# Optimization experiments

Measured on AMD Instinct MI355X. Metric: run time of the kernel, lower is better.

Reference implementation:

```python
import jax, jax.numpy as jnp
import numpy as np

N = 100000  # nodes
E = 320000  # edges
G = 64      # graphs in the batch


def setup_inputs() -> dict:
    key = jax.random.key(0)
    ks = jax.random.split(key, 16)
    inp = {
        "x": jax.random.normal(ks[0], (N, 512), dtype=jnp.float32),
        "edge_index": jax.random.randint(ks[1], (2, E), 0, N, dtype=jnp.int64),
        "batch": jnp.sort(jax.random.randint(ks[2], (N,), 0, G, dtype=jnp.int64)),
    }
    # GCNConv weights (in, out) and biases, Glorot-ish scale
    dims = [(512, 256), (256, 128), (128, 64), (64, 32)]
    for i, (din, dout) in enumerate(dims):
        inp[f"w{i+1}"] = jax.random.normal(ks[3 + i], (din, dout), dtype=jnp.float32) / np.sqrt(din)
        inp[f"b{i+1}"] = jnp.zeros((dout,), dtype=jnp.float32)
    inp["lw1"] = jax.random.normal(ks[8], (32, 16), dtype=jnp.float32) / np.sqrt(32.0)
    inp["lb1"] = jnp.zeros((16,), dtype=jnp.float32)
    inp["lw2"] = jax.random.normal(ks[9], (16, 2), dtype=jnp.float32) / np.sqrt(16.0)
    inp["lb2"] = jnpp = jnp.zeros((2,), dtype=jnp.float32)
    return inp


def _gcn_conv(h_in, w, b, src, dst, norm, n):
    # x' = D^-1/2 (A+I) D^-1/2 (X W) + b   (PyG GCNConv default)
    h = h_in @ w                                  # [N, out]
    msg = h[src] * norm[:, None]                  # gather + scale over edges(+self-loops)
    out = jax.ops.segment_sum(msg, dst, num_segments=n)  # scatter-add
    return out + b


def reference(x, edge_index, batch, w1, b1, w2, b2, w3, b3, w4, b4, lw1, lb1, lw2, lb2):
    n = x.shape[0]
    loop = jnp.arange(n, dtype=edge_index.dtype)
    src = jnp.concatenate([edge_index[0], loop])  # add self-loops
    dst = jnp.concatenate([edge_index[1], loop])
    # symmetric normalization: deg counted at dst (col) including self-loops
    deg = jax.ops.segment_sum(jnp.ones_like(dst, dtype=x.dtype), dst, num_segments=n)
    dinv = jnp.where(deg > 0, 1.0 / jnp.sqrt(deg), 0.0)
    norm = dinv[src] * dinv[dst]                  # [E+N]

    h = jax.nn.relu(_gcn_conv(x, w1, b1, src, dst, norm, n))
    h = jax.nn.relu(_gcn_conv(h, w2, b2, src, dst, norm, n))
    h = jax.nn.relu(_gcn_conv(h, w3, b3, src, dst, norm, n))
    h = _gcn_conv(h, w4, b4, src, dst, norm, n)   # [N, 32]

    # global mean pool over graphs
    sums = jax.ops.segment_sum(h, batch, num_segments=G)
    cnt = jax.ops.segment_sum(jnp.ones((n,), dtype=h.dtype), batch, num_segments=G)
    pooled = sums / jnp.maximum(cnt, 1.0)[:, None]  # [G, 32]

    # dropout p=0.8 is identity in eval mode
    out = jax.nn.relu(pooled @ lw1 + lb1) @ lw2 + lb2  # [G, 2]
    return out
```

## Files before the change

### kernel.cpp

```cpp
#include <hip/hip_runtime.h>
#include <cstdint>
#include <cstddef>


typedef __attribute__((ext_vector_type(8))) short s16x8;
typedef __attribute__((ext_vector_type(4))) float f32x4;

__device__ __forceinline__ short2 split2(float f) {
    union { float f; unsigned u; } c; c.f = f;
    short hi = (short)(c.u >> 16);
    union { unsigned u; float f; } h; h.u = c.u & 0xffff0000u;
    union { float f; unsigned u; } r; r.f = f - h.f;
    short lo = (short)(r.u >> 16);
    return make_short2(hi, lo);
}

__device__ __forceinline__ void gload16(const void* g, void* l) {
    __builtin_amdgcn_global_load_lds(
        (const __attribute__((address_space(1))) unsigned int*)g,
        (__attribute__((address_space(3))) unsigned int*)l, 16, 0, 0);
}


__global__ void k_split_x(const float* __restrict__ x, long total8,
                          unsigned short* __restrict__ xh, unsigned short* __restrict__ xl) {
    long i = (long)blockIdx.x * blockDim.x + threadIdx.x;
    long stride = (long)gridDim.x * blockDim.x;
    for (; i < total8; i += stride) {
        const float4* p = (const float4*)(x + i * 8);
        float4 a = p[0], b = p[1];
        float v[8] = {a.x, a.y, a.z, a.w, b.x, b.y, b.z, b.w};
        s16x8 h, l;
#pragma unroll
        for (int j = 0; j < 8; ++j) { short2 q = split2(v[j]); h[j] = q.x; l[j] = q.y; }
        *(s16x8*)(xh + i * 8) = h;
        *(s16x8*)(xl + i * 8) = l;
    }
}


__global__ void k_count(const int* __restrict__ dst, int E, int* __restrict__ cnt) {
    int e = blockIdx.x * blockDim.x + threadIdx.x;
    if (e < E) atomicAdd(&cnt[dst[e]], 1);
}

__global__ void k_dinv(const int* __restrict__ cnt, int n, float* __restrict__ dinv) {
    int i = blockIdx.x * blockDim.x + threadIdx.x;
    if (i < n) dinv[i] = rsqrtf((float)(cnt[i] + 1));
}

__global__ void k_scan_sums(const int* __restrict__ cnt, int n, int* __restrict__ bsum) {
    __shared__ int s[256];
    int t = threadIdx.x;
    int base = blockIdx.x * 4096 + t * 16;
    int sum = 0;
#pragma unroll
    for (int j = 0; j < 16; ++j) { int i = base + j; if (i < n) sum += cnt[i]; }
    s[t] = sum;
    __syncthreads();
    for (int off = 128; off > 0; off >>= 1) {
        if (t < off) s[t] += s[t + off];
        __syncthreads();
    }
    if (t == 0) bsum[blockIdx.x] = s[0];
}

__global__ void k_scan_offsets(const int* __restrict__ bsum, int nb,
                               int* __restrict__ boff, int* __restrict__ totalp) {
    int t = threadIdx.x;
    int v = (t < nb) ? bsum[t] : 0;
    int x = v;
    for (int off = 1; off < 64; off <<= 1) {
        int y = __shfl_up(x, off);
        if (t >= off) x += y;
    }
    if (t < nb) boff[t] = x - v;
    if (t == 63) *totalp = x;
}

__global__ void k_scan_final(const int* __restrict__ cnt, int n,
                             const int* __restrict__ boff, int* __restrict__ row_ptr) {
    __shared__ int s[256];
    int t = threadIdx.x;
    int base = blockIdx.x * 4096 + t * 16;
    int v[16]; int sum = 0;
#pragma unroll
    for (int j = 0; j < 16; ++j) { int i = base + j; v[j] = (i < n) ? cnt[i] : 0; sum += v[j]; }
    s[t] = sum;
    __syncthreads();
    for (int off = 1; off < 256; off <<= 1) {
        int y = (t >= off) ? s[t - off] : 0;
        __syncthreads();
        s[t] += y;
        __syncthreads();
    }
    int run = boff[blockIdx.x] + ((t == 0) ? 0 : s[t - 1]);
#pragma unroll
    for (int j = 0; j < 16; ++j) {
        int i = base + j;
        if (i < n) row_ptr[i] = run;
        run += v[j];
    }
}

__global__ void k_fill(const int* __restrict__ src, const int* __restrict__ dst, int E,
                       const int* __restrict__ row_ptr, int* __restrict__ cursor,
                       int* __restrict__ csr_src) {
    int e = blockIdx.x * blockDim.x + threadIdx.x;
    if (e >= E) return;
    int d = dst[e];
    int p = atomicAdd(&cursor[d], 1);
    csr_src[row_ptr[d] + p] = src[e];
}


__global__ void k_split_w(const float* __restrict__ w, int N, int total, int kshift,
                          unsigned short* __restrict__ th, unsigned short* __restrict__ tl) {
    int idx = blockIdx.x * blockDim.x + threadIdx.x;
    if (idx >= total) return;
    int nn = idx >> kshift;
    int k  = idx & ((1 << kshift) - 1);
    short2 p = split2(w[(size_t)k * N + nn]);
    th[idx] = (unsigned short)p.x;
    tl[idx] = (unsigned short)p.y;
}


template <int FN>
__global__ __launch_bounds__(256)
void k_gemm(const unsigned short* __restrict__ Ah, const unsigned short* __restrict__ Al,
            const unsigned short* __restrict__ Bth, const unsigned short* __restrict__ Btl,
            float* __restrict__ C, int M, int K, int N) {
    constexpr int FM = 4;
    constexpr int BM = 128;
    constexpr int BN = 2 * FN * 16;
    constexpr int BK = 32;
    __shared__ char sAh[BM * 64], sAl[BM * 64];
    __shared__ char sBh[BN * 64], sBl[BN * 64];

    const int tid  = threadIdx.x;
    const int lane = tid & 63;
    const int w    = tid >> 6;
    const int wm   = w & 1;
    const int wn   = w >> 1;
    const int brow = blockIdx.y * BM;
    const int bcol = blockIdx.x * BN;
    const int l15  = lane & 15;
    const int kb   = (lane >> 4) * 16;

    f32x4 acc[FM][FN];
#pragma unroll
    for (int i = 0; i < FM; ++i)
#pragma unroll
        for (int j = 0; j < FN; ++j) acc[i][j] = (f32x4){0.f, 0.f, 0.f, 0.f};

    const int KT = K / BK;
    for (int t = 0; t < KT; ++t) {
        const int k0 = t * BK;

#pragma unroll
        for (int u = 0; u < 4; ++u) {
            int id = w + u * 4;
            int hi = (id < 8) ? 1 : 0;
            int s  = hi ? id : id - 8;
            int p  = s * 64 + lane;
            int kq = (p ^ ((p >> 3) & 3)) & 3;
            int row = p >> 2;
            const unsigned short* gs = (hi ? Ah : Al) + (size_t)(brow + row) * K + k0 + kq * 8;
            gload16(gs, (hi ? sAh : sAl) + s * 1024);
        }
#pragma unroll
        for (int u = 0; u < BN / 32; ++u) {
            int id = w + u * 4;
            int hi = (id < BN / 16) ? 1 : 0;
            int s  = hi ? id : id - BN / 16;
            int p  = s * 64 + lane;
            int kq = (p ^ ((p >> 3) & 3)) & 3;
            int col = p >> 2;
            const unsigned short* gs = (hi ? Bth : Btl) + (size_t)(bcol + col) * K + k0 + kq * 8;
            gload16(gs, (hi ? sBh : sBl) + s * 1024);
        }
        __syncthreads();

        s16x8 fah[FM], fam[FM];
#pragma unroll
        for (int i = 0; i < FM; ++i) {
            int row = wm * 64 + i * 16 + l15;
            int o = row * 64 + (kb ^ (((row >> 1) & 3) << 4));
            fah[i] = *(const s16x8*)(sAh + o);
            fam[i] = *(const s16x8*)(sAl + o);
        }
#pragma unroll
        for (int j = 0; j < FN; ++j) {
            int col = wn * FN * 16 + j * 16 + l15;
            int o = col * 64 + (kb ^ (((col >> 1) & 3) << 4));
            s16x8 fbh = *(const s16x8*)(sBh + o);
            s16x8 fbm = *(const s16x8*)(sBl + o);
#pragma unroll
            for (int i = 0; i < FM; ++i) {
                acc[i][j] = __builtin_amdgcn_mfma_f32_16x16x32_bf16(fah[i], fbh, acc[i][j], 0, 0, 0);
                acc[i][j] = __builtin_amdgcn_mfma_f32_16x16x32_bf16(fam[i], fbh, acc[i][j], 0, 0, 0);
                acc[i][j] = __builtin_amdgcn_mfma_f32_16x16x32_bf16(fah[i], fbm, acc[i][j], 0, 0, 0);
            }
        }
        __syncthreads();
    }

#pragma unroll
    for (int i = 0; i < FM; ++i) {
#pragma unroll
        for (int r = 0; r < 4; ++r) {
            int row = brow + wm * 64 + i * 16 + (lane >> 4) * 4 + r;
            if (row >= M) continue;
#pragma unroll
            for (int j = 0; j < FN; ++j) {
                int col = bcol + wn * FN * 16 + j * 16 + l15;
                C[(size_t)row * N + col] = acc[i][j][r];
            }
        }
    }
}


__global__ void k_agg_split(const float4* __restrict__ h, const int* __restrict__ row_ptr,
                            const int* __restrict__ csr_src, const float* __restrict__ dinv,
                            const float* __restrict__ bias,
                            unsigned short* __restrict__ oh, unsigned short* __restrict__ ol,
                            int n, int f_shift) {
    int idx = blockIdx.x * blockDim.x + threadIdx.x;
    int dout4 = 1 << f_shift;
    int total = n << f_shift;
    if (idx >= total) return;
    int i = idx >> f_shift;
    int f = idx & (dout4 - 1);

    float di = dinv[i];
    float4 hv = h[(size_t)i * dout4 + f];
    float4 acc;
    acc.x = hv.x * di; acc.y = hv.y * di; acc.z = hv.z * di; acc.w = hv.w * di;

    int s0 = row_ptr[i], s1 = row_ptr[i + 1];
    for (int e = s0; e < s1; ++e) {
        int s = csr_src[e];
        float ds = dinv[s];
        float4 v = h[(size_t)s * dout4 + f];
        acc.x += v.x * ds; acc.y += v.y * ds; acc.z += v.z * ds; acc.w += v.w * ds;
    }
    const float4* b4 = (const float4*)bias;
    float4 b = b4[f];
    float4 o;
    o.x = fmaxf(acc.x * di + b.x, 0.f);
    o.y = fmaxf(acc.y * di + b.y, 0.f);
    o.z = fmaxf(acc.z * di + b.z, 0.f);
    o.w = fmaxf(acc.w * di + b.w, 0.f);

    short2 p0 = split2(o.x), p1 = split2(o.y), p2 = split2(o.z), p3 = split2(o.w);
    size_t base = ((size_t)i << f_shift << 2) + f * 4;
    *(ushort4*)(oh + base) = make_ushort4((unsigned short)p0.x, (unsigned short)p1.x,
                                          (unsigned short)p2.x, (unsigned short)p3.x);
    *(ushort4*)(ol + base) = make_ushort4((unsigned short)p0.y, (unsigned short)p1.y,
                                          (unsigned short)p2.y, (unsigned short)p3.y);
}


__global__ void k_agg(const float4* __restrict__ h, const int* __restrict__ row_ptr,
                      const int* __restrict__ csr_src, const float* __restrict__ dinv,
                      const float* __restrict__ bias, float4* __restrict__ out,
                      int n, int f_shift) {
    int idx = blockIdx.x * blockDim.x + threadIdx.x;
    int dout4 = 1 << f_shift;
    int total = n << f_shift;
    if (idx >= total) return;
    int i = idx >> f_shift;
    int f = idx & (dout4 - 1);

    float di = dinv[i];
    float4 hv = h[(size_t)i * dout4 + f];
    float4 acc;
    acc.x = hv.x * di; acc.y = hv.y * di; acc.z = hv.z * di; acc.w = hv.w * di;

    int s0 = row_ptr[i], s1 = row_ptr[i + 1];
    for (int e = s0; e < s1; ++e) {
        int s = csr_src[e];
        float ds = dinv[s];
        float4 v = h[(size_t)s * dout4 + f];
        acc.x += v.x * ds; acc.y += v.y * ds; acc.z += v.z * ds; acc.w += v.w * ds;
    }
    const float4* b4 = (const float4*)bias;
    float4 b = b4[f];
    float4 o;
    o.x = acc.x * di + b.x;
    o.y = acc.y * di + b.y;
    o.z = acc.z * di + b.z;
    o.w = acc.w * di + b.w;
    out[(size_t)i * dout4 + f] = o;
}


__global__ void k_pool(const float* __restrict__ h, const int* __restrict__ batch,
                       int n, float* __restrict__ pooled) {
    int g = blockIdx.x;
    int start, end;
    {
        int lo = 0, hi = n;
        while (lo < hi) { int mid = (lo + hi) >> 1; if (batch[mid] < g) lo = mid + 1; else hi = mid; }
        start = lo;
        lo = start; hi = n;
        while (lo < hi) { int mid = (lo + hi) >> 1; if (batch[mid] < g + 1) lo = mid + 1; else hi = mid; }
        end = lo;
    }
    int f = threadIdx.x & 31;
    int sub = threadIdx.x >> 5;
    float s = 0.f;
    for (int i = start + sub; i < end; i += 8) s += h[(size_t)i * 32 + f];
    __shared__ float red[8][32];
    red[sub][f] = s;
    __syncthreads();
    if (sub == 0) {
        float t = 0.f;
#pragma unroll
        for (int k = 0; k < 8; ++k) t += red[k][f];
        int c = end - start;
        pooled[g * 32 + f] = t / (float)(c > 0 ? c : 1);
    }
}


__global__ void k_mlp(const float* __restrict__ pooled, const float* __restrict__ lw1,
                      const float* __restrict__ lb1, const float* __restrict__ lw2,
                      const float* __restrict__ lb2, float* __restrict__ out, int g_count) {
    int g = threadIdx.x;
    if (g >= g_count) return;
    float p[32];
#pragma unroll
    for (int k = 0; k < 32; ++k) p[k] = pooled[g * 32 + k];
    float hmid[16];
#pragma unroll
    for (int j = 0; j < 16; ++j) {
        float s = lb1[j];
#pragma unroll
        for (int k = 0; k < 32; ++k) s += p[k] * lw1[k * 16 + j];
        hmid[j] = fmaxf(s, 0.f);
    }
#pragma unroll
    for (int o = 0; o < 2; ++o) {
        float s = lb2[o];
#pragma unroll
        for (int k = 0; k < 16; ++k) s += hmid[k] * lw2[k * 2 + o];
        out[g * 2 + o] = s;
    }
}


extern "C" void kernel_launch(void* const* d_in, const int* in_sizes, int n_in,
                              void* d_out, int out_size, void* d_ws, size_t ws_size,
                              hipStream_t stream) {
    const float* x     = (const float*)d_in[0];
    const int*   ei    = (const int*)d_in[1];
    const int*   batch = (const int*)d_in[2];
    const float* w1 = (const float*)d_in[3];  const float* b1 = (const float*)d_in[4];
    const float* w2 = (const float*)d_in[5];  const float* b2 = (const float*)d_in[6];
    const float* w3 = (const float*)d_in[7];  const float* b3 = (const float*)d_in[8];
    const float* w4 = (const float*)d_in[9];  const float* b4 = (const float*)d_in[10];
    const float* lw1 = (const float*)d_in[11]; const float* lb1 = (const float*)d_in[12];
    const float* lw2 = (const float*)d_in[13]; const float* lb2 = (const float*)d_in[14];
    float* out = (float*)d_out;

    const int n = in_sizes[0] / 512;
    const int E = in_sizes[1] / 2;
    const int G = 64;

    const int* src = ei;
    const int* dst = ei + E;

    char* ws = (char*)d_ws;
    size_t off = 0;
    auto alloc = [&](size_t bytes) -> void* {
        void* p = ws + off;
        off = (off + bytes + 255) & ~((size_t)255);
        return p;
    };
    float*          bufA = (float*)alloc((size_t)n * 256 * sizeof(float));
    unsigned short* xh   = (unsigned short*)alloc((size_t)n * 512 * 2);
    unsigned short* xl   = (unsigned short*)alloc((size_t)n * 512 * 2);
    unsigned short* pAh  = (unsigned short*)alloc((size_t)n * 256 * 2);
    unsigned short* pAl  = (unsigned short*)alloc((size_t)n * 256 * 2);
    int*   cnt     = (int*)alloc((size_t)n * sizeof(int));
    int*   row_ptr = (int*)alloc((size_t)(n + 1) * sizeof(int));
    int*   cursor  = (int*)alloc((size_t)n * sizeof(int));
    int*   csr     = (int*)alloc((size_t)E * sizeof(int));
    float* dinv    = (float*)alloc((size_t)n * sizeof(float));
    float* pooled  = (float*)alloc((size_t)G * 32 * sizeof(float));
    int*   bsum    = (int*)alloc(64 * sizeof(int));
    int*   boff    = (int*)alloc(64 * sizeof(int));
    unsigned short* w1h = (unsigned short*)alloc(256 * 512 * 2);
    unsigned short* w1l = (unsigned short*)alloc(256 * 512 * 2);
    unsigned short* w2h = (unsigned short*)alloc(128 * 256 * 2);
    unsigned short* w2l = (unsigned short*)alloc(128 * 256 * 2);
    unsigned short* w3h = (unsigned short*)alloc(64 * 128 * 2);
    unsigned short* w3l = (unsigned short*)alloc(64 * 128 * 2);
    unsigned short* w4h = (unsigned short*)alloc(32 * 64 * 2);
    unsigned short* w4l = (unsigned short*)alloc(32 * 64 * 2);
    float* bufB = (float*)(pAl + (size_t)n * 64);
    (void)ws_size;

    hipMemsetAsync(cnt, 0, (size_t)n * sizeof(int), stream);
    hipMemsetAsync(cursor, 0, (size_t)n * sizeof(int), stream);

    k_split_x<<<2048, 256, 0, stream>>>(x, (long)n * 64, xh, xl);
    k_split_w<<<(256 * 512 + 255) / 256, 256, 0, stream>>>(w1, 256, 256 * 512, 9, w1h, w1l);
    k_split_w<<<(128 * 256 + 255) / 256, 256, 0, stream>>>(w2, 128, 128 * 256, 8, w2h, w2l);
    k_split_w<<<(64 * 128 + 255) / 256, 256, 0, stream>>>(w3, 64, 64 * 128, 7, w3h, w3l);
    k_split_w<<<(32 * 64 + 255) / 256, 256, 0, stream>>>(w4, 32, 32 * 64, 6, w4h, w4l);

    const int nscan = (n + 4095) / 4096;
    k_count<<<(E + 255) / 256, 256, 0, stream>>>(dst, E, cnt);
    k_dinv <<<(n + 255) / 256, 256, 0, stream>>>(cnt, n, dinv);
    k_scan_sums   <<<nscan, 256, 0, stream>>>(cnt, n, bsum);
    k_scan_offsets<<<1, 64, 0, stream>>>(bsum, nscan, boff, row_ptr + n);
    k_scan_final  <<<nscan, 256, 0, stream>>>(cnt, n, boff, row_ptr);
    k_fill<<<(E + 255) / 256, 256, 0, stream>>>(src, dst, E, row_ptr, cursor, csr);

    const int gy = (n + 127) / 128;

    k_gemm<4><<<dim3(2, gy), 256, 0, stream>>>(xh, xl, w1h, w1l, bufA, n, 512, 256);
    k_agg_split<<<((size_t)n * 64 + 255) / 256, 256, 0, stream>>>(
        (const float4*)bufA, row_ptr, csr, dinv, b1, pAh, pAl, n, 6);

    k_gemm<4><<<dim3(1, gy), 256, 0, stream>>>(pAh, pAl, w2h, w2l, bufA, n, 256, 128);
    k_agg_split<<<((size_t)n * 32 + 255) / 256, 256, 0, stream>>>(
        (const float4*)bufA, row_ptr, csr, dinv, b2, pAh, pAl, n, 5);

    k_gemm<2><<<dim3(1, gy), 256, 0, stream>>>(pAh, pAl, w3h, w3l, bufA, n, 128, 64);
    k_agg_split<<<((size_t)n * 16 + 255) / 256, 256, 0, stream>>>(
        (const float4*)bufA, row_ptr, csr, dinv, b3, pAh, pAl, n, 4);

    k_gemm<1><<<dim3(1, gy), 256, 0, stream>>>(pAh, pAl, w4h, w4l, bufA, n, 64, 32);
    k_agg<<<((size_t)n * 8 + 255) / 256, 256, 0, stream>>>(
        (const float4*)bufA, row_ptr, csr, dinv, b4, (float4*)bufB, n, 3);

    k_pool<<<G, 256, 0, stream>>>(bufB, batch, n, pooled);
    k_mlp<<<1, 64, 0, stream>>>(pooled, lw1, lb1, lw2, lb2, out, G);
}
```

Before: 569.9 us.

## Load GEMM fragments directly from global into registers with double buffering

Replaces the LDS-staged GEMM (global_load_lds plus two __syncthreads per K step) with direct per-lane global loads of MFMA fragments into registers. K is now a template parameter so the loop fully unrolls, and two register buffer sets are rotated so loads for the next steps overlap MFMA work. This removes LDS traffic and barriers, but each wave now reads its own A/B fragments from global, losing cross-wave reuse through shared memory and raising register pressure. Out-of-range rows are clamped to avoid reading past the end of the input.

```diff
diff --git a/kernel.cpp b/kernel.cpp
--- a/kernel.cpp
+++ b/kernel.cpp
@@ -13,12 +13,6 @@
     union { float f; unsigned u; } r; r.f = f - h.f;
     short lo = (short)(r.u >> 16);
     return make_short2(hi, lo);
-}
-
-__device__ __forceinline__ void gload16(const void* g, void* l) {
-    __builtin_amdgcn_global_load_lds(
-        (const __attribute__((address_space(1))) unsigned int*)g,
-        (__attribute__((address_space(3))) unsigned int*)l, 16, 0, 0);
 }
 
 
@@ -126,27 +120,35 @@
 }
 
 
-template <int FN>
+template <int FN, int K_>
 __global__ __launch_bounds__(256)
 void k_gemm(const unsigned short* __restrict__ Ah, const unsigned short* __restrict__ Al,
             const unsigned short* __restrict__ Bth, const unsigned short* __restrict__ Btl,
-            float* __restrict__ C, int M, int K, int N) {
+            float* __restrict__ C, int M, int N) {
     constexpr int FM = 4;
-    constexpr int BM = 128;
-    constexpr int BN = 2 * FN * 16;
-    constexpr int BK = 32;
-    __shared__ char sAh[BM * 64], sAl[BM * 64];
-    __shared__ char sBh[BN * 64], sBl[BN * 64];
-
+    constexpr int KT = K_ / 32;
     const int tid  = threadIdx.x;
     const int lane = tid & 63;
     const int w    = tid >> 6;
     const int wm   = w & 1;
     const int wn   = w >> 1;
-    const int brow = blockIdx.y * BM;
-    const int bcol = blockIdx.x * BN;
+    const int brow = blockIdx.y * 128;
+    const int bcol = blockIdx.x * (FN * 32);
     const int l15  = lane & 15;
-    const int kb   = (lane >> 4) * 16;
+    const int ksl  = (lane >> 4) * 8;
+
+    long aoff[FM], boff[FN];
+#pragma unroll
+    for (int i = 0; i < FM; ++i) {
+        int row = brow + wm * 64 + i * 16 + l15;
+        if (row > M - 1) row = M - 1;
+        aoff[i] = (long)row * K_ + ksl;
+    }
+#pragma unroll
+    for (int j = 0; j < FN; ++j) {
+        int col = bcol + wn * FN * 16 + j * 16 + l15;
+        boff[j] = (long)col * K_ + ksl;
+    }
 
     f32x4 acc[FM][FN];
 #pragma unroll
@@ -154,56 +156,48 @@
 #pragma unroll
         for (int j = 0; j < FN; ++j) acc[i][j] = (f32x4){0.f, 0.f, 0.f, 0.f};
 
-    const int KT = K / BK;
-    for (int t = 0; t < KT; ++t) {
-        const int k0 = t * BK;
-
-#pragma unroll
-        for (int u = 0; u < 4; ++u) {
-            int id = w + u * 4;
-            int hi = (id < 8) ? 1 : 0;
-            int s  = hi ? id : id - 8;
-            int p  = s * 64 + lane;
-            int kq = (p ^ ((p >> 3) & 3)) & 3;
-            int row = p >> 2;
-            const unsigned short* gs = (hi ? Ah : Al) + (size_t)(brow + row) * K + k0 + kq * 8;
-            gload16(gs, (hi ? sAh : sAl) + s * 1024);
+    s16x8 a0h[FM], a0l[FM], a1h[FM], a1l[FM];
+    s16x8 b0h[FN], b0l[FN], b1h[FN], b1l[FN];
+
+    auto loadA = [&](s16x8 (&h)[FM], s16x8 (&l)[FM], int k0) {
+#pragma unroll
+        for (int i = 0; i < FM; ++i) {
+            h[i] = *(const s16x8*)(Ah + aoff[i] + k0);
+            l[i] = *(const s16x8*)(Al + aoff[i] + k0);
         }
-#pragma unroll
-        for (int u = 0; u < BN / 32; ++u) {
-            int id = w + u * 4;
-            int hi = (id < BN / 16) ? 1 : 0;
-            int s  = hi ? id : id - BN / 16;
-            int p  = s * 64 + lane;
-            int kq = (p ^ ((p >> 3) & 3)) & 3;
-            int col = p >> 2;
-            const unsigned short* gs = (hi ? Bth : Btl) + (size_t)(bcol + col) * K + k0 + kq * 8;
-            gload16(gs, (hi ? sBh : sBl) + s * 1024);
+    };
+    auto loadB = [&](s16x8 (&h)[FN], s16x8 (&l)[FN], int k0) {
+#pragma unroll
+        for (int j = 0; j < FN; ++j) {
+            h[j] = *(const s16x8*)(Bth + boff[j] + k0);
+            l[j] = *(const s16x8*)(Btl + boff[j] + k0);
         }
-        __syncthreads();
-
-        s16x8 fah[FM], fam[FM];
-#pragma unroll
-        for (int i = 0; i < FM; ++i) {
-            int row = wm * 64 + i * 16 + l15;
-            int o = row * 64 + (kb ^ (((row >> 1) & 3) << 4));
-            fah[i] = *(const s16x8*)(sAh + o);
-            fam[i] = *(const s16x8*)(sAl + o);
+    };
+    auto stepM = [&](s16x8 (&ah)[FM], s16x8 (&al)[FM], s16x8 (&bh)[FN], s16x8 (&bl)[FN]) {
+#pragma unroll
+        for (int j = 0; j < FN; ++j)
+#pragma unroll
+            for (int i = 0; i < FM; ++i) {
+                acc[i][j] = __builtin_amdgcn_mfma_f32_16x16x32_bf16(ah[i], bh[j], acc[i][j], 0, 0, 0);
+                acc[i][j] = __builtin_amdgcn_mfma_f32_16x16x32_bf16(al[i], bh[j], acc[i][j], 0, 0, 0);
+                acc[i][j] = __builtin_amdgcn_mfma_f32_16x16x32_bf16(ah[i], bl[j], acc[i][j], 0, 0, 0);
+            }
+    };
+
+    loadB(b0h, b0l, 0);
+    loadA(a0h, a0l, 0);
+    if (KT > 1) { loadB(b1h, b1l, 32); loadA(a1h, a1l, 32); }
+
+#pragma unroll
+    for (int t = 0; t < KT; t += 2) {
+        stepM(a0h, a0l, b0h, b0l);
+        if (t + 2 < KT) loadB(b0h, b0l, (t + 2) * 32);
+        stepM(a1h, a1l, b1h, b1l);
+        if (t + 2 < KT) {
+            loadA(a0h, a0l, (t + 2) * 32);
+            loadA(a1h, a1l, (t + 3) * 32);
+            loadB(b1h, b1l, (t + 3) * 32);
         }
-#pragma unroll
-        for (int j = 0; j < FN; ++j) {
-            int col = wn * FN * 16 + j * 16 + l15;
-            int o = col * 64 + (kb ^ (((col >> 1) & 3) << 4));
-            s16x8 fbh = *(const s16x8*)(sBh + o);
-            s16x8 fbm = *(const s16x8*)(sBl + o);
-#pragma unroll
-            for (int i = 0; i < FM; ++i) {
-                acc[i][j] = __builtin_amdgcn_mfma_f32_16x16x32_bf16(fah[i], fbh, acc[i][j], 0, 0, 0);
-                acc[i][j] = __builtin_amdgcn_mfma_f32_16x16x32_bf16(fam[i], fbh, acc[i][j], 0, 0, 0);
-                acc[i][j] = __builtin_amdgcn_mfma_f32_16x16x32_bf16(fah[i], fbm, acc[i][j], 0, 0, 0);
-            }
-        }
-        __syncthreads();
     }
 
 #pragma unroll
@@ -423,19 +417,19 @@
 
     const int gy = (n + 127) / 128;
 
-    k_gemm<4><<<dim3(2, gy), 256, 0, stream>>>(xh, xl, w1h, w1l, bufA, n, 512, 256);
+    k_gemm<4, 512><<<dim3(2, gy), 256, 0, stream>>>(xh, xl, w1h, w1l, bufA, n, 256);
     k_agg_split<<<((size_t)n * 64 + 255) / 256, 256, 0, stream>>>(
         (const float4*)bufA, row_ptr, csr, dinv, b1, pAh, pAl, n, 6);
 
-    k_gemm<4><<<dim3(1, gy), 256, 0, stream>>>(pAh, pAl, w2h, w2l, bufA, n, 256, 128);
+    k_gemm<4, 256><<<dim3(1, gy), 256, 0, stream>>>(pAh, pAl, w2h, w2l, bufA, n, 128);
     k_agg_split<<<((size_t)n * 32 + 255) / 256, 256, 0, stream>>>(
         (const float4*)bufA, row_ptr, csr, dinv, b2, pAh, pAl, n, 5);
 
-    k_gemm<2><<<dim3(1, gy), 256, 0, stream>>>(pAh, pAl, w3h, w3l, bufA, n, 128, 64);
+    k_gemm<2, 128><<<dim3(1, gy), 256, 0, stream>>>(pAh, pAl, w3h, w3l, bufA, n, 64);
     k_agg_split<<<((size_t)n * 16 + 255) / 256, 256, 0, stream>>>(
         (const float4*)bufA, row_ptr, csr, dinv, b3, pAh, pAl, n, 4);
 
-    k_gemm<1><<<dim3(1, gy), 256, 0, stream>>>(pAh, pAl, w4h, w4l, bufA, n, 64, 32);
+    k_gemm<1, 64><<<dim3(1, gy), 256, 0, stream>>>(pAh, pAl, w4h, w4l, bufA, n, 32);
     k_agg<<<((size_t)n * 8 + 255) / 256, 256, 0, stream>>>(
         (const float4*)bufA, row_ptr, csr, dinv, b4, (float4*)bufB, n, 3);
 
```

New measurement: 735.0 us. 1.29x slower.
